# Performance work log

Measured on AMD Instinct MI355X. Metric: run time of the kernel, lower is better.

Reference implementation:

```python
import jax, jax.numpy as jnp
import numpy as np

B, L, H, N, DM = 16, 32768, 64, 16, 32


def setup_inputs() -> dict:
    key = jax.random.key(0)
    ks = jax.random.split(key, 16)
    inp = {}
    inp['x'] = jax.random.normal(ks[0], (B, L, H), dtype=jnp.float32)
    inp['control_parameters'] = jax.random.uniform(ks[1], (B, 2), dtype=jnp.float32)
    inp['W0'] = jax.random.normal(ks[2], (2, DM), dtype=jnp.float32) / np.sqrt(2.0)
    inp['b0'] = jnp.zeros((DM,), dtype=jnp.float32)
    inp['W1'] = jax.random.normal(ks[3], (DM, DM), dtype=jnp.float32) / np.sqrt(DM)
    inp['b1'] = jnp.zeros((DM,), dtype=jnp.float32)
    inp['W2'] = jax.random.normal(ks[4], (DM, DM), dtype=jnp.float32) / np.sqrt(DM)
    inp['b2'] = jnp.zeros((DM,), dtype=jnp.float32)
    # BlockV1 input linear
    inp['W_lin'] = jax.random.normal(ks[5], (H, H), dtype=jnp.float32) / np.sqrt(H)
    inp['b_lin'] = jnp.zeros((H,), dtype=jnp.float32)
    # DSSM / S4D parameters (S4D-Lin init)
    log_dt_min, log_dt_max = np.log(1e-3), np.log(1e-1)
    inp['log_dt'] = (log_dt_min + (log_dt_max - log_dt_min)
                     * jax.random.uniform(ks[6], (H,), dtype=jnp.float32))
    inp['A_re'] = -0.5 * jnp.ones((H, N), dtype=jnp.float32)
    inp['A_im'] = jnp.broadcast_to(np.pi * jnp.arange(N, dtype=jnp.float32), (H, N)).copy()
    inp['C_re'] = jax.random.normal(ks[7], (H, N), dtype=jnp.float32) / np.sqrt(2.0)
    inp['C_im'] = jax.random.normal(ks[8], (H, N), dtype=jnp.float32) / np.sqrt(2.0)
    inp['D'] = jax.random.normal(ks[9], (H,), dtype=jnp.float32)
    # FiLM: Linear(DM, 2*H) -> (gamma, beta)
    inp['W_film'] = jax.random.normal(ks[10], (DM, 2 * H), dtype=jnp.float32) / np.sqrt(DM)
    inp['b_film'] = jnp.zeros((2 * H,), dtype=jnp.float32)
    return inp


def _s4d_kernel(log_dt, A_re, A_im, C_re, C_im, length):
    # Diagonal SSM (S4D) convolution kernel via ZOH discretization.
    dt = jnp.exp(log_dt)[:, None]                      # [H,1]
    A = A_re + 1j * A_im                               # [H,N]
    dtA = dt * A                                       # [H,N]
    C = (C_re + 1j * C_im) * (jnp.exp(dtA) - 1.0) / A  # [H,N]
    t = jnp.arange(length, dtype=jnp.float32)          # [L]
    # Vandermonde: K[h,l] = 2 * Re( sum_n C[h,n] * exp(dtA[h,n])^l )
    vand = jnp.exp(dtA[:, :, None] * t)                # [H,N,L] complex
    return 2.0 * jnp.einsum('hn,hnl->hl', C, vand).real


def reference(x, control_parameters, W0, b0, W1, b1, W2, b2,
              W_lin, b_lin, log_dt, A_re, A_im, C_re, C_im, D,
              W_film, b_film):
    gelu = jax.nn.gelu
    # control-parameter MLP -> conditioning vector [B, DM]
    cond = gelu(control_parameters @ W0 + b0)
    cond = gelu(cond @ W1 + b1)
    cond = gelu(cond @ W2 + b2)
    # BlockV1: Linear + act
    h = gelu(x @ W_lin + b_lin)          # [B,L,H]
    u = jnp.swapaxes(h, 1, 2)            # [B,H,L]
    length = u.shape[-1]
    # S4D global convolution via FFT (linear, non-circular)
    K = _s4d_kernel(log_dt, A_re, A_im, C_re, C_im, length)   # [H,L]
    n = 2 * length
    Kf = jnp.fft.rfft(K, n=n)            # [H, n//2+1]
    uf = jnp.fft.rfft(u, n=n)            # [B,H, n//2+1]
    y = jnp.fft.irfft(uf * Kf, n=n)[..., :length] + D[:, None] * u  # [B,H,L]
    y = jnp.swapaxes(y, 1, 2)            # [B,L,H]
    # FiLM conditioning (no batch norm)
    gb = cond @ W_film + b_film          # [B, 2H]
    g, b = jnp.split(gb, 2, axis=-1)     # [B,H] each
    y = gelu(y * g[:, None, :] + b[:, None, :])
    # side-chain gate: elementwise multiply with input
    return x * y
```

## Files before the change

### kernel.cpp

```cpp
#include <hip/hip_runtime.h>
#include <hip/hip_bf16.h>
#include <math.h>

#define B_ 16
#define L_ 32768
#define H_ 64
#define N_ 16
#define DM_ 32
#define TS_ 16
#define US_ 68

typedef __attribute__((ext_vector_type(8))) short short8;
typedef __attribute__((ext_vector_type(4))) float floatx4;
typedef __attribute__((ext_vector_type(2))) float f32x2;

__device__ __forceinline__ float fast_gelu(float v) {
    float z = fmaf(0.044715f * v, v * v, v) * 0.7978845608028654f;
#if __has_builtin(__builtin_amdgcn_exp2f) && __has_builtin(__builtin_amdgcn_rcpf)
    float e = __builtin_amdgcn_exp2f(z * 2.8853900817779268f);
    float t = 1.0f - 2.0f * __builtin_amdgcn_rcpf(e + 1.0f);
#else
    float t = tanhf(z);
#endif
    return 0.5f * v * (1.0f + t);
}

__device__ __forceinline__ unsigned short bf16_rne(float f) {
    unsigned u = __float_as_uint(f);
    return (unsigned short)((u + 0x7FFFu + ((u >> 16) & 1u)) >> 16);
}
__device__ __forceinline__ float bf16_tof(unsigned short h) {
    return __uint_as_float(((unsigned)h) << 16);
}
__device__ __forceinline__ void cvt8(const float* f, short8* hi, short8* lo) {
    union { unsigned u[4]; short8 s; } Hh, Ll;
    #pragma unroll
    for (int jp = 0; jp < 4; ++jp) {
        unsigned short h0 = bf16_rne(f[2*jp]), h1 = bf16_rne(f[2*jp+1]);
        Hh.u[jp] = (unsigned)h0 | ((unsigned)h1 << 16);
        float l0 = f[2*jp]   - bf16_tof(h0);
        float l1 = f[2*jp+1] - bf16_tof(h1);
        Ll.u[jp] = (unsigned)bf16_rne(l0) | ((unsigned)bf16_rne(l1) << 16);
    }
    *hi = Hh.s; *lo = Ll.s;
}

__device__ __forceinline__ void pk_step(f32x2& s, f32x2 w, f32x2 uv0) {
    f32x2 t;
    asm("v_pk_fma_f32 %0, %1, %2, %3 op_sel:[1,1,0] op_sel_hi:[1,0,1] neg_lo:[1,0,0]"
        : "=v"(t) : "v"(w), "v"(s), "v"(uv0));
    asm("v_pk_fma_f32 %0, %1, %0, %2 op_sel_hi:[0,1,1]"
        : "+v"(s) : "v"(w), "v"(t));
}
__device__ __forceinline__ void pk_acc(f32x2& y, f32x2 c, f32x2 s) {
    asm("v_pk_fma_f32 %0, %1, %2, %0"
        : "+v"(y) : "v"(c), "v"(s));
}

__global__ void cond_film_kernel(const float* __restrict__ cp,
    const float* __restrict__ W0, const float* __restrict__ b0,
    const float* __restrict__ W1, const float* __restrict__ b1,
    const float* __restrict__ W2, const float* __restrict__ b2,
    const float* __restrict__ Wf, const float* __restrict__ bf,
    float* __restrict__ film) {
    __shared__ float ca[B_][DM_];
    __shared__ float cb[B_][DM_];
    int tid = threadIdx.x;
    int b = tid >> 5, j = tid & 31;
    float acc = fmaf(cp[b*2+0], W0[j], fmaf(cp[b*2+1], W0[DM_+j], b0[j]));
    ca[b][j] = fast_gelu(acc);
    __syncthreads();
    acc = b1[j];
    #pragma unroll
    for (int i = 0; i < DM_; ++i) acc = fmaf(ca[b][i], W1[i*DM_+j], acc);
    cb[b][j] = fast_gelu(acc);
    __syncthreads();
    acc = b2[j];
    #pragma unroll
    for (int i = 0; i < DM_; ++i) acc = fmaf(cb[b][i], W2[i*DM_+j], acc);
    float c2 = fast_gelu(acc);
    __syncthreads();
    ca[b][j] = c2;
    __syncthreads();
    #pragma unroll
    for (int t = 0; t < 4; ++t) {
        int k = j + DM_*t;
        float a = bf[k];
        #pragma unroll
        for (int i = 0; i < DM_; ++i) a = fmaf(ca[b][i], Wf[i*2*H_+k], a);
        film[b*2*H_ + k] = a;
    }
}

__global__ void coef_kernel(const float* __restrict__ log_dt,
    const float* __restrict__ A_re, const float* __restrict__ A_im,
    const float* __restrict__ C_re, const float* __restrict__ C_im,
    float* __restrict__ coef, float Tf) {
    int g = blockIdx.x * blockDim.x + threadIdx.x;
    if (g >= H_*N_) return;
    int h = g >> 4, n = g & 15;
    float dt = expf(log_dt[h]);
    float Ar = A_re[h*N_+n], Ai = A_im[h*N_+n];
    float ar = dt*Ar, ai = dt*Ai;
    float er = expf(ar);
    float wr = er * cosf(ai), wi = er * sinf(ai);
    float eT = expf(Tf * ar);
    float aT = Tf * ai;
    float wTr = eT * cosf(aT), wTi = eT * sinf(aT);
    float d  = Ar*Ar + Ai*Ai;
    float nr = wr - 1.0f, ni = wi;
    float qr = (nr*Ar + ni*Ai) / d;
    float qi = (ni*Ar - nr*Ai) / d;
    float Cr = C_re[h*N_+n], Ci = C_im[h*N_+n];
    float cr = 2.0f * (Cr*qr - Ci*qi);
    float ci = 2.0f * (Cr*qi + Ci*qr);
    coef[(n*6+0)*H_+h] = wr;
    coef[(n*6+1)*H_+h] = wi;
    coef[(n*6+2)*H_+h] = wTr;
    coef[(n*6+3)*H_+h] = wTi;
    coef[(n*6+4)*H_+h] = cr;
    coef[(n*6+5)*H_+h] = ci;
}

__global__ void chunk_scan_kernel(float* __restrict__ states,
                                  const float* __restrict__ coef, int Cc) {
    int t = blockIdx.x * blockDim.x + threadIdx.x;
    int h = t & 63, n = (t >> 6) & 15, b = t >> 10;
    float wTr = coef[(n*6+2)*H_+h], wTi = coef[(n*6+3)*H_+h];
    float2* sp = (float2*)states + ((size_t)b*Cc)*N_*H_ + (size_t)n*H_ + h;
    const int stride = N_*H_;
    float car = 0.f, cai = 0.f;
    float2 buf[8];
    #pragma unroll
    for (int i = 0; i < 8; ++i) buf[i] = sp[(size_t)i*stride];
    for (int cg = 0; cg < Cc; cg += 8) {
        float2 nb[8];
        #pragma unroll
        for (int i = 0; i < 8; ++i)
            nb[i] = (cg + 8 + i < Cc) ? sp[(size_t)(cg+8+i)*stride]
                                      : make_float2(0.f, 0.f);
        #pragma unroll
        for (int i = 0; i < 8; ++i) {
            float2 v = buf[i];
            sp[(size_t)(cg+i)*stride] = make_float2(car, cai);
            float nr2 = fmaf(wTr, car, fmaf(-wTi, cai, v.x));
            float ni2 = fmaf(wTr, cai, fmaf( wTi, car, v.y));
            car = nr2; cai = ni2;
            buf[i] = nb[i];
        }
    }
}

template<int PHASE, int CC>
__global__ __launch_bounds__(256, 3)
void gemm_scan_kernel(const float* __restrict__ x,
                      const float* __restrict__ W_lin, const float* __restrict__ b_lin,
                      const float* __restrict__ coef, float* __restrict__ states,
                      const float* __restrict__ D, const float* __restrict__ film,
                      float* __restrict__ out) {
    constexpr int TT = L_/CC;
    __shared__ __align__(16) unsigned short Wf[16*64*8];
    __shared__ float uld[4][TS_*US_];
    __shared__ float xld[(PHASE==3) ? 4*TS_*US_ : 4];
    const int lane = threadIdx.x & 63;
    const int wv   = threadIdx.x >> 6;
    const int q    = blockIdx.x*4 + wv;
    const int b    = q / CC;
    const int c    = q % CC;
    const int m    = lane & 15;
    const int quad = lane >> 4;

    for (int kt = 0; kt < 2; ++kt)
        for (int nt = 0; nt < 4; ++nt) {
            float f[8];
            #pragma unroll
            for (int j = 0; j < 8; ++j)
                f[j] = W_lin[(kt*32 + quad*8 + j)*H_ + nt*16 + m];
            short8 hi, lo;
            cvt8(f, &hi, &lo);
            ((short8*)Wf)[(kt*4 + nt)*64 + lane]     = hi;
            ((short8*)Wf)[((2+kt)*4 + nt)*64 + lane] = lo;
        }

    f32x2 w2[N_], s2[N_], c2[N_];
    float g_ = 0.f, be_ = 0.f, Dh = 0.f;
    #pragma unroll
    for (int n = 0; n < N_; ++n) {
        w2[n].x = coef[(n*6+0)*H_ + lane];
        w2[n].y = coef[(n*6+1)*H_ + lane];
    }
    if (PHASE == 1) {
        #pragma unroll
        for (int n = 0; n < N_; ++n) s2[n] = (f32x2){0.f, 0.f};
    } else {
        #pragma unroll
        for (int n = 0; n < N_; ++n) {
            c2[n].x = coef[(n*6+4)*H_ + lane];
            c2[n].y = coef[(n*6+5)*H_ + lane];
            size_t idx = (((size_t)q*N_ + n)*H_ + lane)*2;
            s2[n] = *(const f32x2*)(states + idx);
        }
        g_  = film[b*2*H_ + lane];
        be_ = film[b*2*H_ + H_ + lane];
        Dh  = D[lane];
    }
    float blv[4];
    #pragma unroll
    for (int nt = 0; nt < 4; ++nt) blv[nt] = b_lin[nt*16 + m];

    const float* xp = x + ((size_t)b*L_ + (size_t)c*TT)*H_;
    float* op = out + ((size_t)b*L_ + (size_t)c*TT)*H_;
    float* myu = uld[wv];
    float* myx = (PHASE==3) ? &xld[wv*TS_*US_] : nullptr;

    for (int s = 0; s < TT/TS_; ++s) {
        const float* xs = xp + s*TS_*H_;
        short8 ah[2], al[2];
        #pragma unroll
        for (int kt = 0; kt < 2; ++kt) {
            const float* src = xs + m*H_ + kt*32 + quad*8;
            float4 v0 = *(const float4*)(src);
            float4 v1 = *(const float4*)(src + 4);
            if (PHASE == 3) {
                float* dst = &myx[m*US_ + kt*32 + quad*8];
                *(float4*)(dst)     = v0;
                *(float4*)(dst + 4) = v1;
            }
            float f[8] = {v0.x, v0.y, v0.z, v0.w, v1.x, v1.y, v1.z, v1.w};
            cvt8(f, &ah[kt], &al[kt]);
        }
        #pragma unroll
        for (int nt = 0; nt < 4; ++nt) {
            floatx4 acc = {0.f, 0.f, 0.f, 0.f};
            #pragma unroll
            for (int kt = 0; kt < 2; ++kt) {
                short8 bh = ((short8*)Wf)[(kt*4 + nt)*64 + lane];
                short8 bl = ((short8*)Wf)[((2+kt)*4 + nt)*64 + lane];
                acc = __builtin_amdgcn_mfma_f32_16x16x32_bf16(ah[kt], bh, acc, 0, 0, 0);
                acc = __builtin_amdgcn_mfma_f32_16x16x32_bf16(al[kt], bh, acc, 0, 0, 0);
                acc = __builtin_amdgcn_mfma_f32_16x16x32_bf16(ah[kt], bl, acc, 0, 0, 0);
            }
            #pragma unroll
            for (int r = 0; r < 4; ++r) {
                int row = quad*4 + r;
                float uv = fast_gelu(acc[r] + blv[nt]);
                myu[row*US_ + nt*16 + m] = uv;
            }
        }
        float uvc = myu[lane];
        float xgc = (PHASE==3) ? myx[lane] : 0.f;
        for (int l = 0; l < TS_; ++l) {
            int ln = (l+1) & (TS_-1);
            float uvn = myu[ln*US_ + lane];
            float xgn = (PHASE==3) ? myx[ln*US_ + lane] : 0.f;
            f32x2 uv0 = {uvc, 0.f};
            if (PHASE == 1) {
                #pragma unroll
                for (int n = 0; n < N_; ++n) pk_step(s2[n], w2[n], uv0);
            } else {
                f32x2 y2 = {0.f, 0.f};
                #pragma unroll
                for (int n = 0; n < N_; ++n) {
                    pk_step(s2[n], w2[n], uv0);
                    pk_acc(y2, c2[n], s2[n]);
                }
                float y  = fmaf(Dh, uvc, y2.x - y2.y);
                float yg = fast_gelu(fmaf(y, g_, be_));
                op[(s*TS_ + l)*H_ + lane] = xgc * yg;
            }
            uvc = uvn; xgc = xgn;
        }
    }
    if (PHASE == 1) {
        #pragma unroll
        for (int n = 0; n < N_; ++n) {
            size_t idx = (((size_t)q*N_ + n)*H_ + lane)*2;
            *(f32x2*)(states + idx) = s2[n];
        }
    }
}

extern "C" void kernel_launch(void* const* d_in, const int* in_sizes, int n_in,
                              void* d_out, int out_size, void* d_ws, size_t ws_size,
                              hipStream_t stream) {
    const float* x     = (const float*)d_in[0];
    const float* cp    = (const float*)d_in[1];
    const float* W0    = (const float*)d_in[2];
    const float* b0    = (const float*)d_in[3];
    const float* W1    = (const float*)d_in[4];
    const float* b1    = (const float*)d_in[5];
    const float* W2    = (const float*)d_in[6];
    const float* b2    = (const float*)d_in[7];
    const float* W_lin = (const float*)d_in[8];
    const float* b_lin = (const float*)d_in[9];
    const float* log_dt= (const float*)d_in[10];
    const float* A_re  = (const float*)d_in[11];
    const float* A_im  = (const float*)d_in[12];
    const float* C_re  = (const float*)d_in[13];
    const float* C_im  = (const float*)d_in[14];
    const float* D     = (const float*)d_in[15];
    const float* W_f   = (const float*)d_in[16];
    const float* b_f   = (const float*)d_in[17];
    float* out = (float*)d_out;

    float* film   = (float*)d_ws;
    float* coef   = film + B_*2*H_;
    float* states = coef + 6*H_*N_;

    cond_film_kernel<<<1, 512, 0, stream>>>(cp, W0, b0, W1, b1, W2, b2,
                                            W_f, b_f, film);

    size_t need64 = (size_t)(B_*2*H_ + 6*H_*N_)*4
                  + (size_t)B_*512*N_*H_*2*4;
    if (ws_size >= need64) {
        coef_kernel<<<4, 256, 0, stream>>>(log_dt, A_re, A_im, C_re, C_im,
                                           coef, 64.0f);
        gemm_scan_kernel<1,512><<<(B_*512)/4, 256, 0, stream>>>(
            x, W_lin, b_lin, coef, states, nullptr, nullptr, nullptr);
        chunk_scan_kernel<<<(B_*N_*H_)/256, 256, 0, stream>>>(states, coef, 512);
        gemm_scan_kernel<3,512><<<(B_*512)/4, 256, 0, stream>>>(
            x, W_lin, b_lin, coef, states, D, film, out);
    } else {
        coef_kernel<<<4, 256, 0, stream>>>(log_dt, A_re, A_im, C_re, C_im,
                                           coef, 128.0f);
        gemm_scan_kernel<1,256><<<(B_*256)/4, 256, 0, stream>>>(
            x, W_lin, b_lin, coef, states, nullptr, nullptr, nullptr);
        chunk_scan_kernel<<<(B_*N_*H_)/256, 256, 0, stream>>>(states, coef, 256);
        gemm_scan_kernel<3,256><<<(B_*256)/4, 256, 0, stream>>>(
            x, W_lin, b_lin, coef, states, D, film, out);
    }
}
```

Before: 500.6 us.

## Prefetch next x tile into registers and drop LDS staging of gate input

Software-pipelines the x loads so the next 16-row tile is fetched into registers while the current tile runs through the MFMA and scan. The gate input for phase 3 is now read directly from global memory into a register array instead of being staged through shared memory. The inner scan loop is fully unrolled, and the launch bound is raised to 4 blocks per SM. The aims are to hide global-load latency and cut LDS traffic and footprint. In exchange, register pressure rises, which could cause spills under the tighter occupancy bound, and x is now read twice from global memory/cache.

```diff
diff --git a/kernel.cpp b/kernel.cpp
--- a/kernel.cpp
+++ b/kernel.cpp
@@ -152,16 +152,16 @@
 }
 
 template<int PHASE, int CC>
-__global__ __launch_bounds__(256, 3)
+__global__ __launch_bounds__(256, 4)
 void gemm_scan_kernel(const float* __restrict__ x,
                       const float* __restrict__ W_lin, const float* __restrict__ b_lin,
                       const float* __restrict__ coef, float* __restrict__ states,
                       const float* __restrict__ D, const float* __restrict__ film,
                       float* __restrict__ out) {
     constexpr int TT = L_/CC;
+    constexpr int NS = TT/TS_;
     __shared__ __align__(16) unsigned short Wf[16*64*8];
     __shared__ float uld[4][TS_*US_];
-    __shared__ float xld[(PHASE==3) ? 4*TS_*US_ : 4];
     const int lane = threadIdx.x & 63;
     const int wv   = threadIdx.x >> 6;
     const int q    = blockIdx.x*4 + wv;
@@ -211,22 +211,36 @@
     const float* xp = x + ((size_t)b*L_ + (size_t)c*TT)*H_;
     float* op = out + ((size_t)b*L_ + (size_t)c*TT)*H_;
     float* myu = uld[wv];
-    float* myx = (PHASE==3) ? &xld[wv*TS_*US_] : nullptr;
-
-    for (int s = 0; s < TT/TS_; ++s) {
+
+    float4 a0[2], a1[2];
+    #pragma unroll
+    for (int kt = 0; kt < 2; ++kt) {
+        const float* src = xp + m*H_ + kt*32 + quad*8;
+        a0[kt] = *(const float4*)(src);
+        a1[kt] = *(const float4*)(src + 4);
+    }
+
+    for (int s = 0; s < NS; ++s) {
         const float* xs = xp + s*TS_*H_;
+        float xg[TS_];
+        if (PHASE == 3) {
+            #pragma unroll
+            for (int l = 0; l < TS_; ++l) xg[l] = xs[l*H_ + lane];
+        }
+        float4 n0[2], n1[2];
+        if (s + 1 < NS) {
+            #pragma unroll
+            for (int kt = 0; kt < 2; ++kt) {
+                const float* src = xs + TS_*H_ + m*H_ + kt*32 + quad*8;
+                n0[kt] = *(const float4*)(src);
+                n1[kt] = *(const float4*)(src + 4);
+            }
+        }
         short8 ah[2], al[2];
         #pragma unroll
         for (int kt = 0; kt < 2; ++kt) {
-            const float* src = xs + m*H_ + kt*32 + quad*8;
-            float4 v0 = *(const float4*)(src);
-            float4 v1 = *(const float4*)(src + 4);
-            if (PHASE == 3) {
-                float* dst = &myx[m*US_ + kt*32 + quad*8];
-                *(float4*)(dst)     = v0;
-                *(float4*)(dst + 4) = v1;
-            }
-            float f[8] = {v0.x, v0.y, v0.z, v0.w, v1.x, v1.y, v1.z, v1.w};
+            float f[8] = {a0[kt].x, a0[kt].y, a0[kt].z, a0[kt].w,
+                          a1[kt].x, a1[kt].y, a1[kt].z, a1[kt].w};
             cvt8(f, &ah[kt], &al[kt]);
         }
         #pragma unroll
@@ -247,13 +261,10 @@
                 myu[row*US_ + nt*16 + m] = uv;
             }
         }
-        float uvc = myu[lane];
-        float xgc = (PHASE==3) ? myx[lane] : 0.f;
+        #pragma unroll
         for (int l = 0; l < TS_; ++l) {
-            int ln = (l+1) & (TS_-1);
-            float uvn = myu[ln*US_ + lane];
-            float xgn = (PHASE==3) ? myx[ln*US_ + lane] : 0.f;
-            f32x2 uv0 = {uvc, 0.f};
+            float uv = myu[l*US_ + lane];
+            f32x2 uv0 = {uv, 0.f};
             if (PHASE == 1) {
                 #pragma unroll
                 for (int n = 0; n < N_; ++n) pk_step(s2[n], w2[n], uv0);
@@ -264,12 +275,13 @@
                     pk_step(s2[n], w2[n], uv0);
                     pk_acc(y2, c2[n], s2[n]);
                 }
-                float y  = fmaf(Dh, uvc, y2.x - y2.y);
+                float y  = fmaf(Dh, uv, y2.x - y2.y);
                 float yg = fast_gelu(fmaf(y, g_, be_));
-                op[(s*TS_ + l)*H_ + lane] = xgc * yg;
+                op[(s*TS_ + l)*H_ + lane] = xg[l] * yg;
             }
-            uvc = uvn; xgc = xgn;
-        }
+        }
+        #pragma unroll
+        for (int kt = 0; kt < 2; ++kt) { a0[kt] = n0[kt]; a1[kt] = n1[kt]; }
     }
     if (PHASE == 1) {
         #pragma unroll
```

After: 656.9 us. +31.2%, slower.

## Split sequential chunk-state scan into three-level hierarchical parallel scan

Applied to the files above, without the earlier changes.

Replaces the single serial carry scan over 512 chunk states per (b,n,h) with a three-phase scan. First, per-group aggregates are computed over 8 groups. Second, a short scan runs across the group aggregates using the decay raised to the group power by repeated squaring. Third, a fix-up pass rewrites the exclusive prefix states inside each group. This gives 8x more threads to the latency-bound serial scan, which had only 16384 threads. The cost is an extra read pass over the states buffer and two more kernel launches.

```diff
diff --git a/kernel.cpp b/kernel.cpp
--- a/kernel.cpp
+++ b/kernel.cpp
@@ -9,6 +9,7 @@
 #define DM_ 32
 #define TS_ 16
 #define US_ 68
+#define NG_ 8
 
 typedef __attribute__((ext_vector_type(8))) short short8;
 typedef __attribute__((ext_vector_type(4))) float floatx4;
@@ -122,23 +123,79 @@
     coef[(n*6+5)*H_+h] = ci;
 }
 
-__global__ void chunk_scan_kernel(float* __restrict__ states,
-                                  const float* __restrict__ coef, int Cc) {
+
+__global__ void scan_agg_kernel(const float* __restrict__ states,
+                                const float* __restrict__ coef,
+                                float* __restrict__ agg, int Cc, int G) {
     int t = blockIdx.x * blockDim.x + threadIdx.x;
-    int h = t & 63, n = (t >> 6) & 15, b = t >> 10;
+    int h = t & 63, n = (t >> 6) & 15, g = (t >> 10) & (NG_-1), b = t >> 13;
     float wTr = coef[(n*6+2)*H_+h], wTi = coef[(n*6+3)*H_+h];
-    float2* sp = (float2*)states + ((size_t)b*Cc)*N_*H_ + (size_t)n*H_ + h;
+    const float2* sp = (const float2*)states
+        + ((size_t)(b*Cc + g*G))*N_*H_ + (size_t)n*H_ + h;
     const int stride = N_*H_;
     float car = 0.f, cai = 0.f;
     float2 buf[8];
     #pragma unroll
     for (int i = 0; i < 8; ++i) buf[i] = sp[(size_t)i*stride];
-    for (int cg = 0; cg < Cc; cg += 8) {
+    for (int cg = 0; cg < G; cg += 8) {
         float2 nb[8];
         #pragma unroll
         for (int i = 0; i < 8; ++i)
-            nb[i] = (cg + 8 + i < Cc) ? sp[(size_t)(cg+8+i)*stride]
-                                      : make_float2(0.f, 0.f);
+            nb[i] = (cg + 8 + i < G) ? sp[(size_t)(cg+8+i)*stride]
+                                     : make_float2(0.f, 0.f);
+        #pragma unroll
+        for (int i = 0; i < 8; ++i) {
+            float2 v = buf[i];
+            float nr2 = fmaf(wTr, car, fmaf(-wTi, cai, v.x));
+            float ni2 = fmaf(wTr, cai, fmaf( wTi, car, v.y));
+            car = nr2; cai = ni2;
+            buf[i] = nb[i];
+        }
+    }
+    ((float2*)agg)[t] = make_float2(car, cai);
+}
+
+__global__ void scan_group_kernel(float* __restrict__ agg,
+                                  const float* __restrict__ coef, int lg2G) {
+    int t = blockIdx.x * blockDim.x + threadIdx.x;
+    int h = t & 63, n = (t >> 6) & 15, b = t >> 10;
+    float wr = coef[(n*6+2)*H_+h], wi = coef[(n*6+3)*H_+h];
+    for (int i = 0; i < lg2G; ++i) {
+        float nr = wr*wr - wi*wi, ni = 2.f*wr*wi;
+        wr = nr; wi = ni;
+    }
+    float car = 0.f, cai = 0.f;
+    float2* ap = (float2*)agg + (size_t)b*NG_*1024 + (size_t)n*64 + h;
+    #pragma unroll
+    for (int g = 0; g < NG_; ++g) {
+        float2 v = ap[(size_t)g*1024];
+        ap[(size_t)g*1024] = make_float2(car, cai);
+        float nr = fmaf(wr, car, fmaf(-wi, cai, v.x));
+        float ni = fmaf(wr, cai, fmaf( wi, car, v.y));
+        car = nr; cai = ni;
+    }
+}
+
+__global__ void scan_fix_kernel(float* __restrict__ states,
+                                const float* __restrict__ coef,
+                                const float* __restrict__ agg, int Cc, int G) {
+    int t = blockIdx.x * blockDim.x + threadIdx.x;
+    int h = t & 63, n = (t >> 6) & 15, g = (t >> 10) & (NG_-1), b = t >> 13;
+    float wTr = coef[(n*6+2)*H_+h], wTi = coef[(n*6+3)*H_+h];
+    float2* sp = (float2*)states
+        + ((size_t)(b*Cc + g*G))*N_*H_ + (size_t)n*H_ + h;
+    const int stride = N_*H_;
+    float2 c0 = ((const float2*)agg)[t];
+    float car = c0.x, cai = c0.y;
+    float2 buf[8];
+    #pragma unroll
+    for (int i = 0; i < 8; ++i) buf[i] = sp[(size_t)i*stride];
+    for (int cg = 0; cg < G; cg += 8) {
+        float2 nb[8];
+        #pragma unroll
+        for (int i = 0; i < 8; ++i)
+            nb[i] = (cg + 8 + i < G) ? sp[(size_t)(cg+8+i)*stride]
+                                     : make_float2(0.f, 0.f);
         #pragma unroll
         for (int i = 0; i < 8; ++i) {
             float2 v = buf[i];
@@ -311,21 +368,34 @@
                                             W_f, b_f, film);
 
     size_t need64 = (size_t)(B_*2*H_ + 6*H_*N_)*4
-                  + (size_t)B_*512*N_*H_*2*4;
+                  + (size_t)B_*512*N_*H_*2*4
+                  + (size_t)B_*NG_*N_*H_*2*4;
     if (ws_size >= need64) {
+        const int Cc = 512, G = 64, lg2G = 6;
+        float* agg = states + (size_t)B_*Cc*N_*H_*2;
         coef_kernel<<<4, 256, 0, stream>>>(log_dt, A_re, A_im, C_re, C_im,
-                                           coef, 64.0f);
+                                           coef, (float)(L_/Cc));
         gemm_scan_kernel<1,512><<<(B_*512)/4, 256, 0, stream>>>(
             x, W_lin, b_lin, coef, states, nullptr, nullptr, nullptr);
-        chunk_scan_kernel<<<(B_*N_*H_)/256, 256, 0, stream>>>(states, coef, 512);
+        scan_agg_kernel<<<(B_*NG_*N_*H_)/256, 256, 0, stream>>>(states, coef,
+                                                                agg, Cc, G);
+        scan_group_kernel<<<(B_*N_*H_)/256, 256, 0, stream>>>(agg, coef, lg2G);
+        scan_fix_kernel<<<(B_*NG_*N_*H_)/256, 256, 0, stream>>>(states, coef,
+                                                                agg, Cc, G);
         gemm_scan_kernel<3,512><<<(B_*512)/4, 256, 0, stream>>>(
             x, W_lin, b_lin, coef, states, D, film, out);
     } else {
+        const int Cc = 256, G = 32, lg2G = 5;
+        float* agg = states + (size_t)B_*Cc*N_*H_*2;
         coef_kernel<<<4, 256, 0, stream>>>(log_dt, A_re, A_im, C_re, C_im,
-                                           coef, 128.0f);
+                                           coef, (float)(L_/Cc));
         gemm_scan_kernel<1,256><<<(B_*256)/4, 256, 0, stream>>>(
             x, W_lin, b_lin, coef, states, nullptr, nullptr, nullptr);
-        chunk_scan_kernel<<<(B_*N_*H_)/256, 256, 0, stream>>>(states, coef, 256);
+        scan_agg_kernel<<<(B_*NG_*N_*H_)/256, 256, 0, stream>>>(states, coef,
+                                                                agg, Cc, G);
+        scan_group_kernel<<<(B_*N_*H_)/256, 256, 0, stream>>>(agg, coef, lg2G);
+        scan_fix_kernel<<<(B_*NG_*N_*H_)/256, 256, 0, stream>>>(states, coef,
+                                                                agg, Cc, G);
         gemm_scan_kernel<3,256><<<(B_*256)/4, 256, 0, stream>>>(
             x, W_lin, b_lin, coef, states, D, film, out);
     }
```

Result: no change. 495.4 us (-1.0%).
